# Performance work log

Measured on AMD Instinct MI355X. Metric: run time of the kernel, lower is better.

The kernel has to match this reference:

```python
import jax, jax.numpy as jnp
import numpy as np

OUT_FEATURES = 512
IN_FEATURES = 512


def _unfold_tt(G1, G2):
    # G1: (1, do0, r, di0), G2: (r, do1, 1, di1)
    # einsum 'abcd,cefg->abefdg' then reshape -> (out_features, in_features)
    W = jnp.einsum('abcd,cefg->abefdg', G1, G2)
    return W.reshape(OUT_FEATURES, IN_FEATURES)


def setup_inputs() -> dict:
    key = jax.random.key(0)
    ks = jax.random.split(key, 5)
    std = np.sqrt(2.0 / IN_FEATURES).astype(np.float32)
    x = jax.random.normal(ks[0], (8, 4096, 2 * IN_FEATURES), dtype=jnp.float32)
    G1_R = jax.random.uniform(ks[1], (1, 32, 4, 32), jnp.float32, -std, std)
    G2_R = jax.random.uniform(ks[2], (4, 16, 1, 16), jnp.float32, -std, std)
    G1_I = jax.random.uniform(ks[3], (1, 32, 4, 32), jnp.float32, -std, std)
    G2_I = jax.random.uniform(ks[4], (4, 16, 1, 16), jnp.float32, -std, std)
    bias_real = jnp.zeros((OUT_FEATURES,), jnp.float32)
    bias_imag = jnp.zeros((OUT_FEATURES,), jnp.float32)
    return {"x": x, "G1_R": G1_R, "G2_R": G2_R, "G1_I": G1_I, "G2_I": G2_I,
            "bias_real": bias_real, "bias_imag": bias_imag}


def reference(x, G1_R, G2_R, G1_I, G2_I, bias_real, bias_imag):
    W_real = _unfold_tt(G1_R, G2_R)  # (out, in)
    W_imag = _unfold_tt(G1_I, G2_I)
    x_real, x_imag = jnp.split(x, 2, axis=-1)
    # F.linear(x, W, b) = x @ W.T + b
    out_real = x_real @ W_real.T - x_imag @ W_imag.T + bias_real
    out_imag = x_real @ W_imag.T + x_imag @ W_real.T + bias_imag
    return jnp.concatenate([out_real, out_imag], axis=-1)
```

## Files before the change

kernel.cpp:

```cpp
#include <hip/hip_runtime.h>
#include <hip/hip_bf16.h>
#include <stdint.h>


typedef _Float16 half8 __attribute__((ext_vector_type(8)));
typedef _Float16 half4v __attribute__((ext_vector_type(4)));
typedef float f32x4 __attribute__((ext_vector_type(4)));

typedef __attribute__((address_space(3))) void* lds_ptr_t;
typedef const __attribute__((address_space(1))) void* gbl_ptr_t;

__device__ __forceinline__ void gload_lds16(const void* g, void* s) {
  __builtin_amdgcn_global_load_lds((gbl_ptr_t)g, (lds_ptr_t)s, 16, 0, 0);
}

#define BARF() asm volatile("s_barrier" ::: "memory")
#define LGKM0() asm volatile("s_waitcnt lgkmcnt(0)" ::: "memory")
#define VMC8() asm volatile("s_waitcnt vmcnt(8)" ::: "memory")
#define VMC0() asm volatile("s_waitcnt vmcnt(0)" ::: "memory")
#define PRIO1() __builtin_amdgcn_s_setprio(1)
#define PRIO0() __builtin_amdgcn_s_setprio(0)


__global__ void build_bt(const float* __restrict__ G1R, const float* __restrict__ G2R,
                         const float* __restrict__ G1I, const float* __restrict__ G2I,
                         _Float16* __restrict__ BTimg) {
  int idx = blockIdx.x * 256 + threadIdx.x;
  int kcol = idx & 63;
  int row  = (idx >> 6) & 255;
  int kt   = (idx >> 14) & 15;
  int nt   = idx >> 18;
  int n = nt * 256 + row;
  int k = kt * 64 + kcol;
  int o = n & 511, i = k & 511;
  bool imagOut = n >= 512, kHi = k >= 512;
  const float* G1; const float* G2; float sign = 1.0f;
  if (imagOut == kHi) { G1 = G1R; G2 = G2R; }
  else { G1 = G1I; G2 = G2I; if (!imagOut) sign = -1.0f; }
  int b = o >> 4, e = o & 15, d = i >> 4, g = i & 15;
  float w = 0.0f;
#pragma unroll
  for (int c = 0; c < 4; ++c)
    w += G1[b * 128 + c * 32 + d] * G2[c * 256 + e * 16 + g];
  size_t byteoff = ((size_t)(nt * 16 + kt) << 15) + (size_t)row * 128
                 + ((kcol * 2) ^ ((row & 7) << 4));
  *(_Float16*)((char*)BTimg + byteoff) = (_Float16)(sign * w);
}

__global__ __launch_bounds__(256) void build_at(const float* __restrict__ A,
                                                _Float16* __restrict__ Aimg) {
  const int tid = threadIdx.x;
  const int kt = blockIdx.x & 15, mt = blockIdx.x >> 4;
  const float* src = A + (size_t)mt * 256 * 1024 + kt * 64;
  char* dst = (char*)Aimg + ((size_t)(mt * 16 + kt) << 15);
  const int cg = tid & 15;
  const int rb = tid >> 4;
#pragma unroll
  for (int r = 0; r < 16; ++r) {
    int row = rb + r * 16;
    float4 v = *(const float4*)(src + (size_t)row * 1024 + cg * 4);
    half4v h = { (_Float16)v.x, (_Float16)v.y, (_Float16)v.z, (_Float16)v.w };
    *(half4v*)(dst + row * 128 + ((cg * 8) ^ ((row & 7) << 4))) = h;
  }
}

__global__ __launch_bounds__(512, 2) void tt_gemm(
    const _Float16* __restrict__ Aimg, const _Float16* __restrict__ Bimg,
    const float* __restrict__ bias_r, const float* __restrict__ bias_i,
    float* __restrict__ C) {
  __shared__ __align__(16) _Float16 Als[2][16384];
  __shared__ __align__(16) _Float16 Bls[2][16384];

  const int tid = threadIdx.x;
  const int bid = blockIdx.x;
  const int bid2 = (bid & 7) * 64 + (bid >> 3);
  const int mt = bid2 >> 2, nt = bid2 & 3;

  const int lane = tid & 63, wid = tid >> 6;
  const int wm = wid >> 2, wn = wid & 3;
  const int lr = lane & 15, lq = lane >> 4;

  f32x4 acc[8][4] = {};
  half8 afr[8][2];
  half8 bfr[4][2];

  const char* Abase = (const char*)Aimg + ((size_t)mt << 19);
  const char* Bbase = (const char*)Bimg + ((size_t)nt << 19);
  const int qoff = wid * 1024 + lane * 16;

  auto stageT = [&](int t, _Float16* Abuf, _Float16* Bbuf) {
    const char* sa = Abase + ((size_t)t << 15) + qoff;
    const char* sb = Bbase + ((size_t)t << 15) + qoff;
#pragma unroll
    for (int q = 0; q < 4; ++q)
      gload_lds16(sa + q * 8192, (char*)Abuf + q * 8192 + wid * 1024);
#pragma unroll
    for (int q = 0; q < 4; ++q)
      gload_lds16(sb + q * 8192, (char*)Bbuf + q * 8192 + wid * 1024);
  };
  auto fragReads = [&](const _Float16* Abuf, const _Float16* Bbuf) {
#pragma unroll
    for (int mf = 0; mf < 8; ++mf)
#pragma unroll
      for (int kk = 0; kk < 2; ++kk) {
        int row = wm * 128 + mf * 16 + lr;
        int byte = row * 128 + ((kk * 64 + lq * 16) ^ ((row & 7) << 4));
        afr[mf][kk] = *(const half8*)((const char*)Abuf + byte);
      }
#pragma unroll
    for (int j = 0; j < 4; ++j)
#pragma unroll
      for (int kk = 0; kk < 2; ++kk) {
        int row = wn * 64 + j * 16 + lr;
        int byte = row * 128 + ((kk * 64 + lq * 16) ^ ((row & 7) << 4));
        bfr[j][kk] = *(const half8*)((const char*)Bbuf + byte);
      }
  };
  auto mmaAll = [&]() {
#pragma unroll
    for (int mf = 0; mf < 8; ++mf)
#pragma unroll
      for (int j = 0; j < 4; ++j)
#pragma unroll
        for (int kk = 0; kk < 2; ++kk)
          acc[mf][j] = __builtin_amdgcn_mfma_f32_16x16x32_f16(
              afr[mf][kk], bfr[j][kk], acc[mf][j], 0, 0, 0);
  };

  stageT(0, Als[0], Bls[0]);
  stageT(1, Als[1], Bls[1]);
  VMC8();
  BARF();

#pragma unroll 2
  for (int t = 0; t < 16; ++t) {
    const int c = t & 1;
    fragReads(Als[c], Bls[c]);
    LGKM0();
    BARF();
    if (t < 14) stageT(t + 2, Als[c], Bls[c]);
    PRIO1(); mmaAll(); PRIO0();
    if (t < 14) { VMC8(); }
    else if (t == 14) { VMC0(); }
    if (t < 15) BARF();
  }

  const int row0 = mt * 256, col0 = nt * 256;
#pragma unroll
  for (int fn = 0; fn < 4; ++fn) {
    int col = col0 + wn * 64 + fn * 16 + lr;
    float bias = (col < 512) ? bias_r[col] : bias_i[col - 512];
#pragma unroll
    for (int fm = 0; fm < 8; ++fm) {
      int r0 = row0 + wm * 128 + fm * 16 + lq * 4;
#pragma unroll
      for (int r = 0; r < 4; ++r)
        C[(size_t)(r0 + r) * 1024 + col] = acc[fm][fn][r] + bias;
    }
  }
}

extern "C" void kernel_launch(void* const* d_in, const int* in_sizes, int n_in,
                              void* d_out, int out_size, void* d_ws, size_t ws_size,
                              hipStream_t stream) {
  const float* x   = (const float*)d_in[0];
  const float* G1R = (const float*)d_in[1];
  const float* G2R = (const float*)d_in[2];
  const float* G1I = (const float*)d_in[3];
  const float* G2I = (const float*)d_in[4];
  const float* br  = (const float*)d_in[5];
  const float* bi  = (const float*)d_in[6];
  float* out = (float*)d_out;

  _Float16* Bimg = (_Float16*)d_ws;
  _Float16* Aimg = (_Float16*)((char*)d_ws + (2u << 20));

  build_bt<<<4096, 256, 0, stream>>>(G1R, G2R, G1I, G2I, Bimg);
  build_at<<<2048, 256, 0, stream>>>(x, Aimg);
  tt_gemm<<<512, 512, 0, stream>>>(Aimg, Bimg, br, bi, out);
}
```

Measured before the change: 130.4 us.

## Split K-tile into halves and overlap LDS fragment reads with MFMA

Fragment loads for each 64-wide K tile are split into two 32-wide halves. The second half is read while the MFMAs for the first half run, and the first half of the next tile is read after the barrier, before the second-half MFMAs. This cuts the main loop from two barriers per iteration to one and hides LDS read latency behind compute. In exchange it waits on all outstanding global loads (vmcnt 0) every iteration and drops the loop unroll pragma, which may expose global load latency and adds dynamic buffer indexing.

```diff
diff --git a/kernel.cpp b/kernel.cpp
--- a/kernel.cpp
+++ b/kernel.cpp
@@ -81,8 +81,7 @@
   const int lr = lane & 15, lq = lane >> 4;
 
   f32x4 acc[8][4] = {};
-  half8 afr[8][2];
-  half8 bfr[4][2];
+  half8 afr0[8], afr1[8], bfr0[4], bfr1[4];
 
   const char* Abase = (const char*)Aimg + ((size_t)mt << 19);
   const char* Bbase = (const char*)Bimg + ((size_t)nt << 19);
@@ -98,51 +97,53 @@
     for (int q = 0; q < 4; ++q)
       gload_lds16(sb + q * 8192, (char*)Bbuf + q * 8192 + wid * 1024);
   };
-  auto fragReads = [&](const _Float16* Abuf, const _Float16* Bbuf) {
+  auto readK0 = [&](const _Float16* Ab, const _Float16* Bb) {
 #pragma unroll
-    for (int mf = 0; mf < 8; ++mf)
+    for (int mf = 0; mf < 8; ++mf) {
+      int row = wm * 128 + mf * 16 + lr;
+      afr0[mf] = *(const half8*)((const char*)Ab + row * 128 + ((lq * 16) ^ ((row & 7) << 4)));
+    }
 #pragma unroll
-      for (int kk = 0; kk < 2; ++kk) {
-        int row = wm * 128 + mf * 16 + lr;
-        int byte = row * 128 + ((kk * 64 + lq * 16) ^ ((row & 7) << 4));
-        afr[mf][kk] = *(const half8*)((const char*)Abuf + byte);
-      }
+    for (int j = 0; j < 4; ++j) {
+      int row = wn * 64 + j * 16 + lr;
+      bfr0[j] = *(const half8*)((const char*)Bb + row * 128 + ((lq * 16) ^ ((row & 7) << 4)));
+    }
+  };
+  auto readK1 = [&](const _Float16* Ab, const _Float16* Bb) {
 #pragma unroll
-    for (int j = 0; j < 4; ++j)
+    for (int mf = 0; mf < 8; ++mf) {
+      int row = wm * 128 + mf * 16 + lr;
+      afr1[mf] = *(const half8*)((const char*)Ab + row * 128 + (((64 + lq * 16) & 127) ^ ((row & 7) << 4)));
+    }
 #pragma unroll
-      for (int kk = 0; kk < 2; ++kk) {
-        int row = wn * 64 + j * 16 + lr;
-        int byte = row * 128 + ((kk * 64 + lq * 16) ^ ((row & 7) << 4));
-        bfr[j][kk] = *(const half8*)((const char*)Bbuf + byte);
-      }
+    for (int j = 0; j < 4; ++j) {
+      int row = wn * 64 + j * 16 + lr;
+      bfr1[j] = *(const half8*)((const char*)Bb + row * 128 + (((64 + lq * 16) & 127) ^ ((row & 7) << 4)));
+    }
   };
-  auto mmaAll = [&]() {
+  auto mmaH = [&](half8 (&af)[8], half8 (&bf)[4]) {
 #pragma unroll
     for (int mf = 0; mf < 8; ++mf)
 #pragma unroll
       for (int j = 0; j < 4; ++j)
-#pragma unroll
-        for (int kk = 0; kk < 2; ++kk)
-          acc[mf][j] = __builtin_amdgcn_mfma_f32_16x16x32_f16(
-              afr[mf][kk], bfr[j][kk], acc[mf][j], 0, 0, 0);
+        acc[mf][j] = __builtin_amdgcn_mfma_f32_16x16x32_f16(
+            af[mf], bf[j], acc[mf][j], 0, 0, 0);
   };
 
   stageT(0, Als[0], Bls[0]);
   stageT(1, Als[1], Bls[1]);
   VMC8();
   BARF();
+  readK0(Als[0], Bls[0]);
 
-#pragma unroll 2
   for (int t = 0; t < 16; ++t) {
     const int c = t & 1;
-    fragReads(Als[c], Bls[c]);
-    LGKM0();
-    BARF();
+    readK1(Als[c], Bls[c]);
+    PRIO1(); mmaH(afr0, bfr0); PRIO0();
+    LGKM0(); VMC0(); BARF();
+    if (t < 15) readK0(Als[c ^ 1], Bls[c ^ 1]);
     if (t < 14) stageT(t + 2, Als[c], Bls[c]);
-    PRIO1(); mmaAll(); PRIO0();
-    if (t < 14) { VMC8(); }
-    else if (t == 14) { VMC0(); }
-    if (t < 15) BARF();
+    PRIO1(); mmaH(afr1, bfr1); PRIO0();
   }
 
   const int row0 = mt * 256, col0 = nt * 256;
```

New measurement: 124.5 us. 4.5% less time.
